# Optimization experiments

Hardware: AMD Instinct MI355X
Metric: run time of the kernel (lower is better)

## Reference

```python
import jax, jax.numpy as jnp
import numpy as np

EPS = 1e-5  # BatchNorm eps
K_NN = 16


def _conv1d(w, b, x):
    # 1x1 Conv1d: w (O,C), x (B,C,N) -> (B,O,N)
    return jnp.einsum('oc,bcn->bon', w, x) + b[None, :, None]


def _conv2d(w, b, x):
    # 1x1 Conv2d: w (O,C), x (B,C,N,K) -> (B,O,N,K)
    return jnp.einsum('oc,bcnk->bonk', w, x) + b[None, :, None, None]


def _bn2d(x, g, bt, mu, var):
    # eval-mode BatchNorm2d over channel axis 1
    inv = g / jnp.sqrt(var + EPS)
    return x * inv[None, :, None, None] + (bt - mu * inv)[None, :, None, None]


def _group(f, idx):
    # grouping_operation: f (B,C,M), idx (B,N,K) -> (B,C,N,K)
    return jax.vmap(lambda fb, ib: fb[:, ib])(f, idx)


def _knn(query_pts, ref_pts, k):
    # query (B,N,3), ref (B,M,3) -> k nearest ref indices per query (B,N,k)
    d = (jnp.sum(query_pts ** 2, -1)[:, :, None]
         + jnp.sum(ref_pts ** 2, -1)[:, None, :]
         - 2.0 * jnp.einsum('bnc,bmc->bnm', query_pts, ref_pts))
    _, idx = jax.lax.top_k(-d, k)
    return idx


def setup_inputs() -> dict:
    key = jax.random.key(0)
    B, n, m, C, D, PH = 4, 4096, 1024, 128, 256, 64
    AH = 2 * D
    ks = iter(jax.random.split(key, 40))

    def nrm(shape, scale):
        return jax.random.normal(next(ks), shape, jnp.float32) * scale

    pos = nrm((B, 3, n), 1.0)
    return {
        'pos': pos,
        'pos_flipped': jnp.transpose(pos, (0, 2, 1)),
        'fea': nrm((B, C, n), 1.0),
        'seed': nrm((B, m, 3), 1.0),
        'seed_fea': nrm((B, C, m), 1.0),
        'w_start': nrm((D, C), C ** -0.5), 'b_start': jnp.zeros((D,), jnp.float32),
        'w_key': nrm((D, D), D ** -0.5), 'b_key': jnp.zeros((D,), jnp.float32),
        'w_value': nrm((D, D), D ** -0.5), 'b_value': jnp.zeros((D,), jnp.float32),
        'w_query': nrm((D, C), C ** -0.5), 'b_query': jnp.zeros((D,), jnp.float32),
        'pos_w1': nrm((PH, 4), 0.5), 'pos_b1': jnp.zeros((PH,), jnp.float32),
        'pos_g1': jnp.ones((PH,), jnp.float32), 'pos_beta1': jnp.zeros((PH,), jnp.float32),
        'pos_mu1': jnp.zeros((PH,), jnp.float32), 'pos_var1': jnp.ones((PH,), jnp.float32),
        'pos_w2': nrm((D, PH), PH ** -0.5), 'pos_b2': jnp.zeros((D,), jnp.float32),
        'attn_w1': nrm((AH, D), D ** -0.5), 'attn_b1': jnp.zeros((AH,), jnp.float32),
        'attn_g1': jnp.ones((AH,), jnp.float32), 'attn_beta1': jnp.zeros((AH,), jnp.float32),
        'attn_mu1': jnp.zeros((AH,), jnp.float32), 'attn_var1': jnp.ones((AH,), jnp.float32),
        'attn_w2': nrm((D, AH), AH ** -0.5), 'attn_b2': jnp.zeros((D,), jnp.float32),
        'w_end': nrm((C, D), D ** -0.5), 'b_end': jnp.zeros((C,), jnp.float32),
    }


def reference(pos, pos_flipped, fea, seed, seed_fea,
              w_start, b_start, w_key, b_key, w_value, b_value, w_query, b_query,
              pos_w1, pos_b1, pos_g1, pos_beta1, pos_mu1, pos_var1, pos_w2, pos_b2,
              attn_w1, attn_b1, attn_g1, attn_beta1, attn_mu1, attn_var1, attn_w2, attn_b2,
              w_end, b_end):
    value = _conv1d(w_start, b_start, seed_fea)                    # (B,D,m)
    idx = _knn(jax.lax.stop_gradient(pos_flipped),
               jax.lax.stop_gradient(seed), K_NN)                  # (B,n,K) no-grad topk
    key_f = _conv1d(w_key, b_key, value)
    val_f = _conv1d(w_value, b_value, value)
    query = _conv1d(w_query, b_query, fea)                         # (B,D,n)
    key_g = _group(key_f, idx)                                     # (B,D,n,K)
    qk_rel = query[:, :, :, None] - key_g
    val_g = _group(val_f, idx)                                     # (B,D,n,K)
    coord_xj = _group(jnp.transpose(seed, (0, 2, 1)), idx)         # (B,3,n,K)
    pos_rel = pos[:, :, :, None] - coord_xj                        # (B,3,n,K)
    dis = jnp.linalg.norm(pos_rel, axis=1, keepdims=True)          # (B,1,n,K)
    h = jnp.concatenate([dis, pos_rel], axis=1)                    # (B,4,n,K)
    pe = _conv2d(pos_w2, pos_b2,
                 jax.nn.relu(_bn2d(_conv2d(pos_w1, pos_b1, h),
                                   pos_g1, pos_beta1, pos_mu1, pos_var1)))  # (B,D,n,K)
    hid = jax.nn.relu(_bn2d(_conv2d(attn_w1, attn_b1, qk_rel + pe),
                            attn_g1, attn_beta1, attn_mu1, attn_var1))
    weights = jax.nn.softmax(_conv2d(attn_w2, attn_b2, hid), axis=-1)  # softmax over K
    agg = jnp.einsum('bcnk,bcnk->bcn', weights, val_g + pe)        # (B,D,n)
    return _conv1d(w_end, b_end, agg) + fea                        # (B,C,n)
```

## Files before the change

### kernel.cpp

```cpp
#include <hip/hip_runtime.h>
#include <hip/hip_bf16.h>

#define BB   4
#define NQ   4096
#define MS   1024
#define CF   128
#define DD   256
#define PHH  64
#define AHH  512
#define KNN  16
#define EPSBN 1e-5f
#define LDT  264
#define LDH  72

typedef unsigned short ushort_t;
typedef __attribute__((ext_vector_type(8))) short bf16x8;
typedef __attribute__((ext_vector_type(4))) float floatx4;

__device__ __forceinline__ float u2f(ushort_t u) {
  return __uint_as_float(((unsigned int)u) << 16);
}
__device__ __forceinline__ ushort_t f2u(float f) {
  __hip_bfloat16 h = __float2bfloat16(f);
  return *(ushort_t*)&h;
}

#define NSEG 30
struct CvtArgs {
  const void* src[NSEG];
  int cnt[NSEG];
  int off[NSEG];
};

__global__ __launch_bounds__(256) void cvt_kernel(CvtArgs a, float* __restrict__ dst,
                                                  const ushort_t* __restrict__ probe) {
  const bool f32 = (probe[0] == 0);
  const int gid = blockIdx.x * 256 + threadIdx.x;
  const int gsz = gridDim.x * 256;
  for (int s = 0; s < NSEG; ++s) {
    float* d = dst + a.off[s];
    const int n = a.cnt[s];
    if (f32) {
      const float* sp = (const float*)a.src[s];
      for (int i = gid; i < n; i += gsz) d[i] = sp[i];
    } else {
      const ushort_t* sp = (const ushort_t*)a.src[s];
      for (int i = gid; i < n; i += gsz) d[i] = u2f(sp[i]);
    }
  }
}

__global__ __launch_bounds__(256) void cvtw_kernel(
    const float* __restrict__ w1f, const float* __restrict__ w2f,
    const float* __restrict__ w2pf, const float* __restrict__ wqf,
    ushort_t* __restrict__ w1b, ushort_t* __restrict__ w2b,
    ushort_t* __restrict__ w2pb, ushort_t* __restrict__ wqtb) {
  int i = blockIdx.x * 256 + threadIdx.x;
  w1b[i] = f2u(w1f[i]);
  w2b[i] = f2u(w2f[i]);
  if (i < DD * PHH) w2pb[i] = f2u(w2pf[i]);
  if (i < CF * DD) {
    int c = i >> 8, d = i & 255;
    wqtb[i] = f2u(wqf[d * CF + c]);
  }
}

__global__ __launch_bounds__(256) void vkv_kernel(
    const float* __restrict__ w_start, const float* __restrict__ b_start,
    const float* __restrict__ w_key, const float* __restrict__ b_key,
    const float* __restrict__ w_value, const float* __restrict__ b_value,
    const float* __restrict__ seed_fea,
    ushort_t* __restrict__ key_b, ushort_t* __restrict__ val_b) {
  __shared__ __align__(16) float s_val[4][DD];
  const int tid = threadIdx.x;
  const int b = blockIdx.x >> 8;
  const int m0 = (blockIdx.x & 255) << 2;

  float a0 = b_start[tid], a1 = a0, a2 = a0, a3 = a0;
  {
    const float* wrow = w_start + tid * CF;
    const float* colb = seed_fea + b * CF * MS + m0;
    for (int c = 0; c < CF; c += 4) {
      float4 w = *(const float4*)(wrow + c);
      float4 f0 = *(const float4*)(colb + (c + 0) * MS);
      float4 f1 = *(const float4*)(colb + (c + 1) * MS);
      float4 f2 = *(const float4*)(colb + (c + 2) * MS);
      float4 f3 = *(const float4*)(colb + (c + 3) * MS);
      a0 += w.x * f0.x + w.y * f1.x + w.z * f2.x + w.w * f3.x;
      a1 += w.x * f0.y + w.y * f1.y + w.z * f2.y + w.w * f3.y;
      a2 += w.x * f0.z + w.y * f1.z + w.z * f2.z + w.w * f3.z;
      a3 += w.x * f0.w + w.y * f1.w + w.z * f2.w + w.w * f3.w;
    }
  }
  s_val[0][tid] = a0; s_val[1][tid] = a1; s_val[2][tid] = a2; s_val[3][tid] = a3;
  __syncthreads();

  float ak[4], av[4];
#pragma unroll
  for (int i = 0; i < 4; ++i) { ak[i] = b_key[tid]; av[i] = b_value[tid]; }
  {
    const float* kr = w_key + tid * DD;
    const float* vr = w_value + tid * DD;
    for (int c = 0; c < DD; c += 4) {
      float4 ku = *(const float4*)(kr + c);
      float4 vu = *(const float4*)(vr + c);
      float4 v0 = *(const float4*)(&s_val[0][c]);
      float4 v1 = *(const float4*)(&s_val[1][c]);
      float4 v2 = *(const float4*)(&s_val[2][c]);
      float4 v3 = *(const float4*)(&s_val[3][c]);
      ak[0] += ku.x * v0.x + ku.y * v0.y + ku.z * v0.z + ku.w * v0.w;
      ak[1] += ku.x * v1.x + ku.y * v1.y + ku.z * v1.z + ku.w * v1.w;
      ak[2] += ku.x * v2.x + ku.y * v2.y + ku.z * v2.z + ku.w * v2.w;
      ak[3] += ku.x * v3.x + ku.y * v3.y + ku.z * v3.z + ku.w * v3.w;
      av[0] += vu.x * v0.x + vu.y * v0.y + vu.z * v0.z + vu.w * v0.w;
      av[1] += vu.x * v1.x + vu.y * v1.y + vu.z * v1.z + vu.w * v1.w;
      av[2] += vu.x * v2.x + vu.y * v2.y + vu.z * v2.z + vu.w * v2.w;
      av[3] += vu.x * v3.x + vu.y * v3.y + vu.z * v3.z + vu.w * v3.w;
    }
  }
#pragma unroll
  for (int i = 0; i < 4; ++i) {
    key_b[(b * MS + m0 + i) * DD + tid] = f2u(ak[i]);
    val_b[(b * MS + m0 + i) * DD + tid] = f2u(av[i]);
  }
}

__global__ __launch_bounds__(256) void knn_kernel(
    const float* __restrict__ pos_flipped, const float* __restrict__ seed,
    int* __restrict__ idx_out) {
  __shared__ float s_x[MS], s_y[MS], s_z[MS], s_r2[MS];
  const int tid = threadIdx.x;
  const int wv = tid >> 6, ln = tid & 63;
  const int b = blockIdx.x >> 10;
  const int q = ((blockIdx.x & 1023) << 2) + wv;

  for (int i = tid; i < MS; i += 256) {
    float x = seed[(b * MS + i) * 3 + 0];
    float y = seed[(b * MS + i) * 3 + 1];
    float z = seed[(b * MS + i) * 3 + 2];
    s_x[i] = x; s_y[i] = y; s_z[i] = z;
    s_r2[i] = x * x + y * y + z * z;
  }
  __syncthreads();

  const float qx = pos_flipped[(b * NQ + q) * 3 + 0];
  const float qy = pos_flipped[(b * NQ + q) * 3 + 1];
  const float qz = pos_flipped[(b * NQ + q) * 3 + 2];
  const float q2 = qx * qx + qy * qy + qz * qz;

  unsigned long long key[16];
#pragma unroll
  for (int t = 0; t < 16; ++t) {
    int j = ln + (t << 6);
    float dist = q2 + s_r2[j] - 2.0f * (qx * s_x[j] + qy * s_y[j] + qz * s_z[j]);
    unsigned u = __float_as_uint(dist);
    u ^= (u >> 31) ? 0xFFFFFFFFu : 0x80000000u;
    key[t] = ((unsigned long long)u << 10) | (unsigned)j;
  }

#pragma unroll 1
  for (int r = 0; r < KNN; ++r) {
    unsigned long long m = key[0];
#pragma unroll
    for (int t = 1; t < 16; ++t) m = (key[t] < m) ? key[t] : m;
#pragma unroll
    for (int off = 32; off >= 1; off >>= 1) {
      unsigned lo = (unsigned)m, hi = (unsigned)(m >> 32);
      unsigned olo = __shfl_xor((int)lo, off);
      unsigned ohi = __shfl_xor((int)hi, off);
      unsigned long long o = ((unsigned long long)ohi << 32) | olo;
      m = (o < m) ? o : m;
    }
    if (ln == 0) idx_out[(b * NQ + q) * KNN + r] = (int)(m & 1023u);
#pragma unroll
    for (int t = 0; t < 16; ++t) key[t] = (key[t] == m) ? ~0ull : key[t];
  }
}

__global__ __launch_bounds__(256, 2) void fused_kernel(
    const float* __restrict__ pos, const float* __restrict__ seed,
    const void* __restrict__ fea_raw,
    const ushort_t* __restrict__ wqtb, const float* __restrict__ b_query,
    const float* __restrict__ pos_w1, const float* __restrict__ pos_b1,
    const float* __restrict__ pos_g1, const float* __restrict__ pos_beta1,
    const float* __restrict__ pos_mu1, const float* __restrict__ pos_var1,
    const ushort_t* __restrict__ w2pb, const float* __restrict__ pos_b2,
    const float* __restrict__ attn_b1, const float* __restrict__ attn_g1,
    const float* __restrict__ attn_beta1, const float* __restrict__ attn_mu1,
    const float* __restrict__ attn_var1,
    const ushort_t* __restrict__ w1b, const ushort_t* __restrict__ w2b,
    const ushort_t* __restrict__ key_b, const ushort_t* __restrict__ val_b,
    const int* __restrict__ idx_in,
    const float* __restrict__ w_end, const float* __restrict__ b_end,
    void* __restrict__ out_raw, const ushort_t* __restrict__ probe) {
  __shared__ __align__(16) ushort_t s_t[64 * LDT];
  __shared__ __align__(16) ushort_t s_phb[64 * LDH];
  __shared__ __align__(16) ushort_t s_hid[64 * LDH];
  __shared__ __align__(16) float s_q[4 * DD];
  __shared__ __align__(16) float s_agg[4 * DD];
  __shared__ float s_h[64 * 4];
  __shared__ int s_idx[64];

  const int tid = threadIdx.x;
  const int wv = tid >> 6;
  const int ln = tid & 63;
  const int qu = ln >> 4, l15 = ln & 15;
  const bool f32io = (probe[0] == 0);
  const int q0 = blockIdx.x * 4;
  const int b = q0 >> 12;
  const int qn0 = q0 & (NQ - 1);

  if (tid < 64) {
    const int g = tid >> 4;
    const int qn = qn0 + g;
    const int j = idx_in[(q0 + g) * KNN + (tid & 15)];
    s_idx[tid] = j;
    float px = pos[(b * 3 + 0) * NQ + qn];
    float py = pos[(b * 3 + 1) * NQ + qn];
    float pz = pos[(b * 3 + 2) * NQ + qn];
    float rx = px - seed[(b * MS + j) * 3 + 0];
    float ry = py - seed[(b * MS + j) * 3 + 1];
    float rz = pz - seed[(b * MS + j) * 3 + 2];
    float dis = sqrtf(rx * rx + ry * ry + rz * rz);
    s_h[tid * 4 + 0] = dis;
    s_h[tid * 4 + 1] = rx;
    s_h[tid * 4 + 2] = ry;
    s_h[tid * 4 + 3] = rz;
  }
  __syncthreads();

  {
    const int p = tid & 63, kb = tid >> 6;
    float4 w = *(const float4*)(pos_w1 + p * 4);
    float inv = pos_g1[p] * rsqrtf(pos_var1[p] + EPSBN);
    float off = pos_b1[p] * inv + pos_beta1[p] - pos_mu1[p] * inv;
#pragma unroll
    for (int i = 0; i < 16; ++i) {
      int gk = kb * 16 + i;
      float raw = w.x * s_h[gk * 4 + 0] + w.y * s_h[gk * 4 + 1] +
                  w.z * s_h[gk * 4 + 2] + w.w * s_h[gk * 4 + 3];
      s_phb[gk * LDH + p] = f2u(fmaxf(raw * inv + off, 0.0f));
    }
  }

  {
    const int d = tid;
    float qd0 = b_query[d], qd1 = qd0, qd2 = qd0, qd3 = qd0;
    const ushort_t* wq = wqtb + d;
    if (f32io) {
      const float* fc = (const float*)fea_raw + (size_t)b * CF * NQ + qn0;
#pragma unroll 4
      for (int c = 0; c < CF; ++c) {
        float w0 = u2f(wq[c * DD]);
        float4 f0 = *(const float4*)(fc + c * NQ);
        qd0 += w0 * f0.x; qd1 += w0 * f0.y;
        qd2 += w0 * f0.z; qd3 += w0 * f0.w;
      }
    } else {
      const ushort_t* fc = (const ushort_t*)fea_raw + (size_t)b * CF * NQ + qn0;
#pragma unroll 4
      for (int c = 0; c < CF; ++c) {
        float w0 = u2f(wq[c * DD]);
        unsigned long long v = *(const unsigned long long*)(fc + c * NQ);
        qd0 += w0 * u2f((ushort_t)(v));
        qd1 += w0 * u2f((ushort_t)(v >> 16));
        qd2 += w0 * u2f((ushort_t)(v >> 32));
        qd3 += w0 * u2f((ushort_t)(v >> 48));
      }
    }
    s_q[0 * DD + d] = qd0; s_q[1 * DD + d] = qd1;
    s_q[2 * DD + d] = qd2; s_q[3 * DD + d] = qd3;
  }
  __syncthreads();

  {
    floatx4 accp[4][4];
#pragma unroll
    for (int mt = 0; mt < 4; ++mt)
#pragma unroll
      for (int nt = 0; nt < 4; ++nt) accp[mt][nt] = (floatx4){0.f, 0.f, 0.f, 0.f};
#pragma unroll
    for (int ks = 0; ks < 2; ++ks) {
      bf16x8 af[4];
#pragma unroll
      for (int mt = 0; mt < 4; ++mt)
        af[mt] = *(const bf16x8*)(s_phb + (mt * 16 + l15) * LDH + ks * 32 + qu * 8);
#pragma unroll
      for (int nt = 0; nt < 4; ++nt) {
        const int d = wv * 64 + nt * 16 + l15;
        bf16x8 bfr = *(const bf16x8*)(w2pb + d * PHH + ks * 32 + qu * 8);
#pragma unroll
        for (int mt = 0; mt < 4; ++mt)
          accp[mt][nt] = __builtin_amdgcn_mfma_f32_16x16x32_bf16(af[mt], bfr, accp[mt][nt], 0, 0, 0);
      }
    }
#pragma unroll
    for (int mt = 0; mt < 4; ++mt) {
#pragma unroll
      for (int nt = 0; nt < 4; ++nt) {
        const int d = wv * 64 + nt * 16 + l15;
        const float qd = s_q[mt * DD + d];
        const float b2v = pos_b2[d];
#pragma unroll
        for (int r = 0; r < 4; ++r) {
          const int row = mt * 16 + qu * 4 + r;
          const int j = s_idx[row];
          float pe = accp[mt][nt][r] + b2v;
          float kf = u2f(key_b[(b * MS + j) * DD + d]);
          s_t[row * LDT + d] = f2u(qd - kf + pe);
        }
      }
    }
  }
  __syncthreads();

  floatx4 accl[4][4];
#pragma unroll
  for (int mt = 0; mt < 4; ++mt)
#pragma unroll
    for (int nt = 0; nt < 4; ++nt) accl[mt][nt] = (floatx4){0.f, 0.f, 0.f, 0.f};

#pragma unroll 1
  for (int nc = 0; nc < 8; ++nc) {
    {
      floatx4 accb[4];
#pragma unroll
      for (int mt = 0; mt < 4; ++mt) accb[mt] = (floatx4){0.f, 0.f, 0.f, 0.f};
#pragma unroll
      for (int ks = 0; ks < 8; ++ks) {
        bf16x8 bfr = *(const bf16x8*)(w1b + (nc * 64 + wv * 16 + l15) * DD + ks * 32 + qu * 8);
#pragma unroll
        for (int mt = 0; mt < 4; ++mt) {
          bf16x8 af = *(const bf16x8*)(s_t + (mt * 16 + l15) * LDT + ks * 32 + qu * 8);
          accb[mt] = __builtin_amdgcn_mfma_f32_16x16x32_bf16(af, bfr, accb[mt], 0, 0, 0);
        }
      }
      const int a = nc * 64 + wv * 16 + l15;
      const int al = wv * 16 + l15;
      float inv = attn_g1[a] * rsqrtf(attn_var1[a] + EPSBN);
      float off = attn_b1[a] * inv + attn_beta1[a] - attn_mu1[a] * inv;
#pragma unroll
      for (int mt = 0; mt < 4; ++mt)
#pragma unroll
        for (int r = 0; r < 4; ++r) {
          const int row = mt * 16 + qu * 4 + r;
          s_hid[row * LDH + al] = f2u(fmaxf(accb[mt][r] * inv + off, 0.0f));
        }
    }
    __syncthreads();
    {
#pragma unroll
      for (int ks = 0; ks < 2; ++ks) {
        bf16x8 af[4];
#pragma unroll
        for (int mt = 0; mt < 4; ++mt)
          af[mt] = *(const bf16x8*)(s_hid + (mt * 16 + l15) * LDH + ks * 32 + qu * 8);
#pragma unroll
        for (int nt = 0; nt < 4; ++nt) {
          bf16x8 bfr = *(const bf16x8*)(w2b + (wv * 64 + nt * 16 + l15) * AHH +
                                        nc * 64 + ks * 32 + qu * 8);
#pragma unroll
          for (int mt = 0; mt < 4; ++mt)
            accl[mt][nt] = __builtin_amdgcn_mfma_f32_16x16x32_bf16(af[mt], bfr, accl[mt][nt], 0, 0, 0);
        }
      }
    }
    __syncthreads();
  }

#pragma unroll
  for (int nt = 0; nt < 4; ++nt) {
    const int c = wv * 64 + nt * 16 + l15;
    floatx4 ap[4];
#pragma unroll
    for (int mt = 0; mt < 4; ++mt) ap[mt] = (floatx4){0.f, 0.f, 0.f, 0.f};
#pragma unroll
    for (int ks = 0; ks < 2; ++ks) {
      bf16x8 bfr = *(const bf16x8*)(w2pb + c * PHH + ks * 32 + qu * 8);
#pragma unroll
      for (int mt = 0; mt < 4; ++mt) {
        bf16x8 af = *(const bf16x8*)(s_phb + (mt * 16 + l15) * LDH + ks * 32 + qu * 8);
        ap[mt] = __builtin_amdgcn_mfma_f32_16x16x32_bf16(af, bfr, ap[mt], 0, 0, 0);
      }
    }
    const float b2v = pos_b2[c];
#pragma unroll
    for (int mt = 0; mt < 4; ++mt) {
      float l0 = accl[mt][nt][0], l1 = accl[mt][nt][1];
      float l2 = accl[mt][nt][2], l3 = accl[mt][nt][3];
      float mx = fmaxf(fmaxf(l0, l1), fmaxf(l2, l3));
      mx = fmaxf(mx, __shfl_xor(mx, 16));
      mx = fmaxf(mx, __shfl_xor(mx, 32));
      float e0 = expf(l0 - mx), e1 = expf(l1 - mx);
      float e2 = expf(l2 - mx), e3 = expf(l3 - mx);
      float s = e0 + e1 + e2 + e3;
      s += __shfl_xor(s, 16);
      s += __shfl_xor(s, 32);
      const int row0 = mt * 16 + qu * 4;
      float v0 = u2f(val_b[(b * MS + s_idx[row0 + 0]) * DD + c]);
      float v1 = u2f(val_b[(b * MS + s_idx[row0 + 1]) * DD + c]);
      float v2 = u2f(val_b[(b * MS + s_idx[row0 + 2]) * DD + c]);
      float v3 = u2f(val_b[(b * MS + s_idx[row0 + 3]) * DD + c]);
      float p = e0 * (v0 + ap[mt][0] + b2v) + e1 * (v1 + ap[mt][1] + b2v) +
                e2 * (v2 + ap[mt][2] + b2v) + e3 * (v3 + ap[mt][3] + b2v);
      p += __shfl_xor(p, 16);
      p += __shfl_xor(p, 32);
      if (ln < 16) s_agg[mt * DD + c] = p / s;
    }
  }
  __syncthreads();

  {
    const int c = tid & 127;
    const int qh = tid >> 7;
    float acc0 = 0.0f, acc1 = 0.0f;
    const float* wr = w_end + c * DD;
    for (int d = 0; d < DD; d += 4) {
      float4 w4 = *(const float4*)(wr + d);
      float4 a0 = *(const float4*)(s_agg + (qh + 0) * DD + d);
      float4 a1 = *(const float4*)(s_agg + (qh + 2) * DD + d);
      acc0 += w4.x * a0.x + w4.y * a0.y + w4.z * a0.z + w4.w * a0.w;
      acc1 += w4.x * a1.x + w4.y * a1.y + w4.z * a1.z + w4.w * a1.w;
    }
    const float be = b_end[c];
#pragma unroll
    for (int t = 0; t < 2; ++t) {
      const int q = qh + t * 2;
      const float accv = (t == 0) ? acc0 : acc1;
      const int oidx = (b * CF + c) * NQ + qn0 + q;
      float fres = f32io ? ((const float*)fea_raw)[oidx]
                         : u2f(((const ushort_t*)fea_raw)[oidx]);
      float v = accv + be + fres;
      if (f32io) ((float*)out_raw)[oidx] = v;
      else ((ushort_t*)out_raw)[oidx] = f2u(v);
    }
  }
}

extern "C" void kernel_launch(void* const* d_in, const int* in_sizes, int n_in,
                              void* d_out, int out_size, void* d_ws, size_t ws_size,
                              hipStream_t stream) {
  (void)in_sizes; (void)n_in; (void)out_size; (void)ws_size;

  float* wsf = (float*)d_ws;
  ushort_t* key_b = (ushort_t*)wsf;
  ushort_t* val_b = (ushort_t*)(wsf + 524288);
  int*      idxw  = (int*)(wsf + 1048576);
  float*    nrm   = wsf + 1310720;
  ushort_t* w1b   = (ushort_t*)(wsf + 2458304);
  ushort_t* w2b   = (ushort_t*)(wsf + 2523840);
  ushort_t* w2pb  = (ushort_t*)(wsf + 2589376);
  ushort_t* wqtb  = (ushort_t*)(wsf + 2597568);

  static const int seg_in[NSEG] = {0, 1, 3, 4, 5, 6, 7, 8, 9, 10, 11, 12, 13, 14,
                                   15, 16, 17, 18, 19, 20, 21, 22, 23, 24, 25, 26,
                                   27, 28, 29, 30};
  static const int seg_cnt[NSEG] = {
      49152, 49152, 12288, 524288, 32768, 256, 65536, 256, 65536, 256,
      32768, 256, 256, 64, 64, 64, 64, 64, 16384, 256,
      131072, 512, 512, 512, 512, 512, 131072, 256, 32768, 128};
  static const int seg_off[NSEG] = {
      0, 49152, 98304, 110592, 634880, 667648, 667904, 733440, 733696, 799232,
      799488, 832256, 832512, 832768, 832832, 832896, 832960, 833024, 833088, 849472,
      849728, 980800, 981312, 981824, 982336, 982848, 983360, 1114432, 1114688, 1147456};

  CvtArgs ca;
  for (int s = 0; s < NSEG; ++s) {
    ca.src[s] = d_in[seg_in[s]];
    ca.cnt[s] = seg_cnt[s];
    ca.off[s] = seg_off[s];
  }
  const ushort_t* probe = (const ushort_t*)d_in[18];

  const float* posN      = nrm + 0;
  const float* pos_flipN = nrm + 49152;
  const float* seedN     = nrm + 98304;
  const float* seed_feaN = nrm + 110592;
  const float* w_startN  = nrm + 634880;
  const float* b_startN  = nrm + 667648;
  const float* w_keyN    = nrm + 667904;
  const float* b_keyN    = nrm + 733440;
  const float* w_valueN  = nrm + 733696;
  const float* b_valueN  = nrm + 799232;
  const float* b_queryN  = nrm + 832256;
  const float* pos_w1N   = nrm + 832512;
  const float* pos_b1N   = nrm + 832768;
  const float* pos_g1N   = nrm + 832832;
  const float* pos_beta1N= nrm + 832896;
  const float* pos_mu1N  = nrm + 832960;
  const float* pos_var1N = nrm + 833024;
  const float* pos_w2N   = nrm + 833088;
  const float* pos_b2N   = nrm + 849472;
  const float* attn_w1N  = nrm + 849728;
  const float* attn_b1N  = nrm + 980800;
  const float* attn_g1N  = nrm + 981312;
  const float* attn_beta1N = nrm + 981824;
  const float* attn_mu1N = nrm + 982336;
  const float* attn_var1N= nrm + 982848;
  const float* attn_w2N  = nrm + 983360;
  const float* w_endN    = nrm + 1114688;
  const float* b_endN    = nrm + 1147456;
  const float* w_queryN  = nrm + 799488;

  cvt_kernel<<<512, 256, 0, stream>>>(ca, nrm, probe);
  cvtw_kernel<<<512, 256, 0, stream>>>(attn_w1N, attn_w2N, pos_w2N, w_queryN,
                                       w1b, w2b, w2pb, wqtb);
  vkv_kernel<<<BB * MS / 4, 256, 0, stream>>>(w_startN, b_startN, w_keyN, b_keyN,
                                              w_valueN, b_valueN, seed_feaN,
                                              key_b, val_b);
  knn_kernel<<<BB * NQ / 4, 256, 0, stream>>>(pos_flipN, seedN, idxw);

  fused_kernel<<<BB * NQ / 4, 256, 0, stream>>>(
      posN, seedN, d_in[2], wqtb, b_queryN,
      pos_w1N, pos_b1N, pos_g1N, pos_beta1N, pos_mu1N, pos_var1N,
      w2pb, pos_b2N,
      attn_b1N, attn_g1N, attn_beta1N, attn_mu1N, attn_var1N,
      w1b, w2b, key_b, val_b, idxw,
      w_endN, b_endN, d_out, probe);
}
```

Baseline: 800.6 us.

## Stage gathered key/value rows in LDS, cache pos-embedding, raise occupancy

Gathered key and value rows are now copied into shared memory with 16-byte vector loads, replacing per-element scattered global reads. The position-embedding output is packed to bf16 and kept in registers rather than recomputed with MFMAs in the epilogue. The first attention GEMM is re-tiled so each wave keeps its A fragments in registers. Shared buffers are merged to cut LDS use, and launch bounds ask for 3 blocks per CU. This trades extra register pressure, possible spills, and bf16 rounding of the position embedding for fewer global gathers and less redundant compute.

New measurement: 1.178 ms. 47.2% more time.

```diff
diff --git a/kernel.cpp b/kernel.cpp
--- a/kernel.cpp
+++ b/kernel.cpp
@@ -23,6 +23,9 @@
 __device__ __forceinline__ ushort_t f2u(float f) {
   __hip_bfloat16 h = __float2bfloat16(f);
   return *(ushort_t*)&h;
+}
+__device__ __forceinline__ unsigned pk2(float a, float b) {
+  return (unsigned)f2u(a) | ((unsigned)f2u(b) << 16);
 }
 
 #define NSEG 30
@@ -177,7 +180,7 @@
   }
 }
 
-__global__ __launch_bounds__(256, 2) void fused_kernel(
+__global__ __launch_bounds__(256, 3) void fused_kernel(
     const float* __restrict__ pos, const float* __restrict__ seed,
     const void* __restrict__ fea_raw,
     const ushort_t* __restrict__ wqtb, const float* __restrict__ b_query,
@@ -194,10 +197,8 @@
     const float* __restrict__ w_end, const float* __restrict__ b_end,
     void* __restrict__ out_raw, const ushort_t* __restrict__ probe) {
   __shared__ __align__(16) ushort_t s_t[64 * LDT];
-  __shared__ __align__(16) ushort_t s_phb[64 * LDH];
-  __shared__ __align__(16) ushort_t s_hid[64 * LDH];
-  __shared__ __align__(16) float s_q[4 * DD];
-  __shared__ __align__(16) float s_agg[4 * DD];
+  __shared__ __align__(16) ushort_t s_pb[64 * LDH];
+  __shared__ __align__(16) float s_qa[4 * DD];
   __shared__ float s_h[64 * 4];
   __shared__ int s_idx[64];
 
@@ -230,6 +231,15 @@
   __syncthreads();
 
   {
+    const int vrow = tid >> 2, vc0 = (tid & 3) * 8;
+    const ushort_t* src = key_b + (b * MS + s_idx[vrow]) * DD + vc0;
+    ushort_t* dst = s_t + vrow * LDT + vc0;
+#pragma unroll
+    for (int i = 0; i < 8; ++i)
+      *(bf16x8*)(dst + i * 32) = *(const bf16x8*)(src + i * 32);
+  }
+
+  {
     const int p = tid & 63, kb = tid >> 6;
     float4 w = *(const float4*)(pos_w1 + p * 4);
     float inv = pos_g1[p] * rsqrtf(pos_var1[p] + EPSBN);
@@ -239,7 +249,7 @@
       int gk = kb * 16 + i;
       float raw = w.x * s_h[gk * 4 + 0] + w.y * s_h[gk * 4 + 1] +
                   w.z * s_h[gk * 4 + 2] + w.w * s_h[gk * 4 + 3];
-      s_phb[gk * LDH + p] = f2u(fmaxf(raw * inv + off, 0.0f));
+      s_pb[gk * LDH + p] = f2u(fmaxf(raw * inv + off, 0.0f));
     }
   }
 
@@ -268,11 +278,12 @@
         qd3 += w0 * u2f((ushort_t)(v >> 48));
       }
     }
-    s_q[0 * DD + d] = qd0; s_q[1 * DD + d] = qd1;
-    s_q[2 * DD + d] = qd2; s_q[3 * DD + d] = qd3;
-  }
-  __syncthreads();
-
+    s_qa[0 * DD + d] = qd0; s_qa[1 * DD + d] = qd1;
+    s_qa[2 * DD + d] = qd2; s_qa[3 * DD + d] = qd3;
+  }
+  __syncthreads();
+
+  unsigned ppk[4][4][2];
   {
     floatx4 accp[4][4];
 #pragma unroll
@@ -284,7 +295,7 @@
       bf16x8 af[4];
 #pragma unroll
       for (int mt = 0; mt < 4; ++mt)
-        af[mt] = *(const bf16x8*)(s_phb + (mt * 16 + l15) * LDH + ks * 32 + qu * 8);
+        af[mt] = *(const bf16x8*)(s_pb + (mt * 16 + l15) * LDH + ks * 32 + qu * 8);
 #pragma unroll
       for (int nt = 0; nt < 4; ++nt) {
         const int d = wv * 64 + nt * 16 + l15;
@@ -299,20 +310,37 @@
 #pragma unroll
       for (int nt = 0; nt < 4; ++nt) {
         const int d = wv * 64 + nt * 16 + l15;
-        const float qd = s_q[mt * DD + d];
+        const float qd = s_qa[mt * DD + d];
         const float b2v = pos_b2[d];
+        float pe[4];
 #pragma unroll
         for (int r = 0; r < 4; ++r) {
           const int row = mt * 16 + qu * 4 + r;
-          const int j = s_idx[row];
-          float pe = accp[mt][nt][r] + b2v;
-          float kf = u2f(key_b[(b * MS + j) * DD + d]);
-          s_t[row * LDT + d] = f2u(qd - kf + pe);
+          pe[r] = accp[mt][nt][r] + b2v;
+          float kf = u2f(s_t[row * LDT + d]);
+          s_t[row * LDT + d] = f2u(qd - kf + pe[r]);
         }
-      }
-    }
-  }
-  __syncthreads();
+        ppk[mt][nt][0] = pk2(pe[0], pe[1]);
+        ppk[mt][nt][1] = pk2(pe[2], pe[3]);
+      }
+    }
+  }
+  __syncthreads();
+
+  bf16x8 afr[8];
+#pragma unroll
+  for (int ks = 0; ks < 8; ++ks)
+    afr[ks] = *(const bf16x8*)(s_t + (wv * 16 + l15) * LDT + ks * 32 + qu * 8);
+  __syncthreads();
+
+  {
+    const int vrow = tid >> 2, vc0 = (tid & 3) * 8;
+    const ushort_t* src = val_b + (b * MS + s_idx[vrow]) * DD + vc0;
+    ushort_t* dst = s_t + vrow * LDT + vc0;
+#pragma unroll
+    for (int i = 0; i < 8; ++i)
+      *(bf16x8*)(dst + i * 32) = *(const bf16x8*)(src + i * 32);
+  }
 
   floatx4 accl[4][4];
 #pragma unroll
@@ -325,43 +353,42 @@
     {
       floatx4 accb[4];
 #pragma unroll
-      for (int mt = 0; mt < 4; ++mt) accb[mt] = (floatx4){0.f, 0.f, 0.f, 0.f};
+      for (int nt = 0; nt < 4; ++nt) accb[nt] = (floatx4){0.f, 0.f, 0.f, 0.f};
 #pragma unroll
       for (int ks = 0; ks < 8; ++ks) {
-        bf16x8 bfr = *(const bf16x8*)(w1b + (nc * 64 + wv * 16 + l15) * DD + ks * 32 + qu * 8);
-#pragma unroll
-        for (int mt = 0; mt < 4; ++mt) {
-          bf16x8 af = *(const bf16x8*)(s_t + (mt * 16 + l15) * LDT + ks * 32 + qu * 8);
-          accb[mt] = __builtin_amdgcn_mfma_f32_16x16x32_bf16(af, bfr, accb[mt], 0, 0, 0);
+#pragma unroll
+        for (int nt = 0; nt < 4; ++nt) {
+          bf16x8 bfr = *(const bf16x8*)(w1b + (nc * 64 + nt * 16 + l15) * DD + ks * 32 + qu * 8);
+          accb[nt] = __builtin_amdgcn_mfma_f32_16x16x32_bf16(afr[ks], bfr, accb[nt], 0, 0, 0);
         }
       }
-      const int a = nc * 64 + wv * 16 + l15;
-      const int al = wv * 16 + l15;
-      float inv = attn_g1[a] * rsqrtf(attn_var1[a] + EPSBN);
-      float off = attn_b1[a] * inv + attn_beta1[a] - attn_mu1[a] * inv;
-#pragma unroll
-      for (int mt = 0; mt < 4; ++mt)
+#pragma unroll
+      for (int nt = 0; nt < 4; ++nt) {
+        const int a = nc * 64 + nt * 16 + l15;
+        float inv = attn_g1[a] * rsqrtf(attn_var1[a] + EPSBN);
+        float off = attn_b1[a] * inv + attn_beta1[a] - attn_mu1[a] * inv;
 #pragma unroll
         for (int r = 0; r < 4; ++r) {
-          const int row = mt * 16 + qu * 4 + r;
-          s_hid[row * LDH + al] = f2u(fmaxf(accb[mt][r] * inv + off, 0.0f));
+          const int row = wv * 16 + qu * 4 + r;
+          s_pb[row * LDH + nt * 16 + l15] = f2u(fmaxf(accb[nt][r] * inv + off, 0.0f));
         }
+      }
     }
     __syncthreads();
     {
 #pragma unroll
       for (int ks = 0; ks < 2; ++ks) {
-        bf16x8 af[4];
+        bf16x8 af2[4];
 #pragma unroll
         for (int mt = 0; mt < 4; ++mt)
-          af[mt] = *(const bf16x8*)(s_hid + (mt * 16 + l15) * LDH + ks * 32 + qu * 8);
+          af2[mt] = *(const bf16x8*)(s_pb + (mt * 16 + l15) * LDH + ks * 32 + qu * 8);
 #pragma unroll
         for (int nt = 0; nt < 4; ++nt) {
           bf16x8 bfr = *(const bf16x8*)(w2b + (wv * 64 + nt * 16 + l15) * AHH +
                                         nc * 64 + ks * 32 + qu * 8);
 #pragma unroll
           for (int mt = 0; mt < 4; ++mt)
-            accl[mt][nt] = __builtin_amdgcn_mfma_f32_16x16x32_bf16(af[mt], bfr, accl[mt][nt], 0, 0, 0);
+            accl[mt][nt] = __builtin_amdgcn_mfma_f32_16x16x32_bf16(af2[mt], bfr, accl[mt][nt], 0, 0, 0);
         }
       }
     }
@@ -371,19 +398,6 @@
 #pragma unroll
   for (int nt = 0; nt < 4; ++nt) {
     const int c = wv * 64 + nt * 16 + l15;
-    floatx4 ap[4];
-#pragma unroll
-    for (int mt = 0; mt < 4; ++mt) ap[mt] = (floatx4){0.f, 0.f, 0.f, 0.f};
-#pragma unroll
-    for (int ks = 0; ks < 2; ++ks) {
-      bf16x8 bfr = *(const bf16x8*)(w2pb + c * PHH + ks * 32 + qu * 8);
-#pragma unroll
-      for (int mt = 0; mt < 4; ++mt) {
-        bf16x8 af = *(const bf16x8*)(s_phb + (mt * 16 + l15) * LDH + ks * 32 + qu * 8);
-        ap[mt] = __builtin_amdgcn_mfma_f32_16x16x32_bf16(af, bfr, ap[mt], 0, 0, 0);
-      }
-    }
-    const float b2v = pos_b2[c];
 #pragma unroll
     for (int mt = 0; mt < 4; ++mt) {
       float l0 = accl[mt][nt][0], l1 = accl[mt][nt][1];
@@ -397,15 +411,19 @@
       s += __shfl_xor(s, 16);
       s += __shfl_xor(s, 32);
       const int row0 = mt * 16 + qu * 4;
-      float v0 = u2f(val_b[(b * MS + s_idx[row0 + 0]) * DD + c]);
-      float v1 = u2f(val_b[(b * MS + s_idx[row0 + 1]) * DD + c]);
-      float v2 = u2f(val_b[(b * MS + s_idx[row0 + 2]) * DD + c]);
-      float v3 = u2f(val_b[(b * MS + s_idx[row0 + 3]) * DD + c]);
-      float p = e0 * (v0 + ap[mt][0] + b2v) + e1 * (v1 + ap[mt][1] + b2v) +
-                e2 * (v2 + ap[mt][2] + b2v) + e3 * (v3 + ap[mt][3] + b2v);
+      float v0 = u2f(s_t[(row0 + 0) * LDT + c]);
+      float v1 = u2f(s_t[(row0 + 1) * LDT + c]);
+      float v2 = u2f(s_t[(row0 + 2) * LDT + c]);
+      float v3 = u2f(s_t[(row0 + 3) * LDT + c]);
+      float pe0 = u2f((ushort_t)(ppk[mt][nt][0] & 0xFFFFu));
+      float pe1 = u2f((ushort_t)(ppk[mt][nt][0] >> 16));
+      float pe2 = u2f((ushort_t)(ppk[mt][nt][1] & 0xFFFFu));
+      float pe3 = u2f((ushort_t)(ppk[mt][nt][1] >> 16));
+      float p = e0 * (v0 + pe0) + e1 * (v1 + pe1) +
+                e2 * (v2 + pe2) + e3 * (v3 + pe3);
       p += __shfl_xor(p, 16);
       p += __shfl_xor(p, 32);
-      if (ln < 16) s_agg[mt * DD + c] = p / s;
+      if (ln < 16) s_qa[mt * DD + c] = p / s;
     }
   }
   __syncthreads();
@@ -417,8 +435,8 @@
     const float* wr = w_end + c * DD;
     for (int d = 0; d < DD; d += 4) {
       float4 w4 = *(const float4*)(wr + d);
-      float4 a0 = *(const float4*)(s_agg + (qh + 0) * DD + d);
-      float4 a1 = *(const float4*)(s_agg + (qh + 2) * DD + d);
+      float4 a0 = *(const float4*)(s_qa + (qh + 0) * DD + d);
+      float4 a1 = *(const float4*)(s_qa + (qh + 2) * DD + d);
       acc0 += w4.x * a0.x + w4.y * a0.y + w4.z * a0.z + w4.w * a0.w;
       acc1 += w4.x * a1.x + w4.y * a1.y + w4.z * a1.z + w4.w * a1.w;
     }
```
